# Optimization experiments

Measured on AMD Instinct MI355X. Metric: run time of the kernel, lower is better.

The kernel has to match this reference:

```python
import jax, jax.numpy as jnp
import numpy as np

NQ, NS, QN, SN = 10000, 500, 4, 10   # num_question, num_skill, q/s neighbor sizes
B, S, D = 32, 200, 128               # batch, seq_len, emb_dim
HOPS = 3


def setup_inputs() -> dict:
    key = jax.random.key(0)
    ks = iter(jax.random.split(key, 40))

    def nrm(shape, scale=0.05):
        return jax.random.normal(next(ks), shape, dtype=jnp.float32) * scale

    return {
        "question": jax.random.randint(next(ks), (B, S), 0, NQ),
        "response": jax.random.randint(next(ks), (B, S), 0, 2),
        "mask": jnp.ones((B, S), dtype=jnp.int32),
        "q_neighbors": jax.random.randint(next(ks), (NQ, QN), 0, NS),  # question -> skill ids
        "s_neighbors": jax.random.randint(next(ks), (NS, SN), 0, NQ),  # skill -> question ids
        "qs_skills": jax.random.randint(next(ks), (NQ, 4), 0, NS),     # related skills per question
        "emb_q": nrm((NQ, D), 1.0),
        "emb_s": nrm((NS, D), 1.0),
        "emb_r": nrm((2, D), 1.0),
        "W_ih": nrm((2 * D, 4 * D)), "b_ih": nrm((4 * D,)), "b_hh": nrm((4 * D,)),
        "ft_W": nrm((D, D)), "ft_b": nrm((D,)),
        "agg_W": nrm((HOPS, D, D)), "agg_b": nrm((HOPS, D)),
        "last_W": nrm((D, D)), "last_b": nrm((D,)),
        "q_W": nrm((D, D)), "q_b": nrm((D,)),
        "k_W": nrm((D, D)), "k_b": nrm((D,)),
        "w_W": nrm((2 * D,)), "w_b": nrm(()),
    }


def reference(question, response, mask, q_neighbors, s_neighbors, qs_skills,
              emb_q, emb_s, emb_r, W_ih, b_ih, b_hh, ft_W, ft_b,
              agg_W, agg_b, last_W, last_b, q_W, q_b, k_W, k_b, w_W, w_b):
    # ---- multi-hop GNN aggregation for every (b, t) question (mask == 1 everywhere) ----
    q_flat = question.reshape(-1)              # [B*S]
    lvl1 = q_neighbors[q_flat]                 # [N, QN]            skill ids
    lvl2 = s_neighbors[lvl1]                   # [N, QN, SN]        question ids
    lvl3 = q_neighbors[lvl2]                   # [N, QN, SN, QN]    skill ids
    embs = [emb_q[q_flat], emb_s[lvl1], emb_q[lvl2], emb_s[lvl3]]
    for i in range(HOPS):
        embs = [jnp.tanh((embs[j] + embs[j + 1].mean(axis=-2)) @ agg_W[j] + agg_b[j])
                for j in range(HOPS - i)]
    agg_emb = jnp.tanh(embs[0] @ last_W + last_b).reshape(B, S, D)

    # ---- per-step input + zero-state LSTMCell (source calls lstm_cell without hx) ----
    q_trans = jax.nn.relu(agg_emb @ ft_W + ft_b)
    x = jnp.concatenate([q_trans, emb_r[response]], axis=-1)   # [B, S, 2D]
    gates = x @ W_ih + b_ih + b_hh                             # h_prev = 0, c_prev = 0
    i_g, f_g, g_g, o_g = jnp.split(gates, 4, axis=-1)
    c = jax.nn.sigmoid(i_g) * jnp.tanh(g_g)
    h = jax.nn.sigmoid(o_g) * jnp.tanh(c)                      # [B, S, D]
    states = h[:, :S - 1]                                      # state written at step t

    # ---- soft-recap attention prediction for q_next = question[:, t+1] ----
    q_next = question[:, 1:]                                   # [B, T], T = S-1
    qs = jnp.concatenate([emb_q[q_next][:, :, None, :], emb_s[qs_skills[q_next]]], axis=2)  # [B,T,5,D]

    inner = jnp.einsum('bnd,btmd->btnm', states, qs)           # state/qs inner products
    a_state = (states @ q_W + q_b) @ w_W[:D]                   # [B, N]  MLP_query on states
    a_qs = (qs @ k_W + k_b) @ w_W[D:]                          # [B, T, 5] MLP_key on qs
    logits = a_state[:, None, :, None] + a_qs[:, :, None, :] + w_b  # [B, T, N, 5]

    t_idx = jnp.arange(S - 1)
    valid = t_idx[None, :] <= t_idx[:, None]                   # [T, N]: states 0..t visible at t
    logits = jnp.where(valid[None, :, :, None], logits, -jnp.inf)
    alpha = jax.nn.softmax(logits.reshape(B, S - 1, -1), axis=-1).reshape(logits.shape)
    pred = jnp.sum(alpha * jax.nn.sigmoid(inner), axis=(2, 3))  # [B, T]

    return jnp.zeros((B, S), jnp.float32).at[:, 1:].set(pred)
```

## Files before the change

kernel.cpp:

```cpp
#include <hip/hip_runtime.h>

typedef unsigned short u16;
typedef unsigned int   u32;

#define NQd 10000
#define NSd 500
#define Bd  32
#define Sd  200
#define Td  199
#define Dd  128
#define NR  6368
#define PB  208

typedef __attribute__((ext_vector_type(8))) short bf16x8;
typedef __attribute__((ext_vector_type(4))) float f32x4;

__device__ __forceinline__ float sigf(float x) {
  return __builtin_amdgcn_rcpf(1.f + __expf(-x));
}
__device__ __forceinline__ float tanh_f(float x) {
  float ax = fminf(fabsf(x), 15.f);
  float e = __expf(2.f * ax);
  float r = 1.f - 2.f * __builtin_amdgcn_rcpf(e + 1.f);
  return copysignf(r, x);
}
__device__ __forceinline__ float bf2f(u16 u) { return __uint_as_float(((u32)u) << 16); }
__device__ __forceinline__ u16 f2bf(float f) {
  u32 b = __float_as_uint(f);
  b += 0x7FFFu + ((b >> 16) & 1u);
  return (u16)(b >> 16);
}
__device__ __forceinline__ float rnd(float x) { return bf2f(f2bf(x)); }
__device__ __forceinline__ void unp2(u32 u, float &a, float &b) {
  a = __uint_as_float(u << 16);
  b = __uint_as_float(u & 0xffff0000u);
}
__device__ __forceinline__ void unpack16(uint4 a0, uint4 a1, float* f) {
  unp2(a0.x, f[0], f[1]);  unp2(a0.y, f[2], f[3]);
  unp2(a0.z, f[4], f[5]);  unp2(a0.w, f[6], f[7]);
  unp2(a1.x, f[8], f[9]);  unp2(a1.y, f[10], f[11]);
  unp2(a1.z, f[12], f[13]); unp2(a1.w, f[14], f[15]);
}

struct Args {
  const int *question, *response, *q_nb, *s_nb, *qs_sk;
  const float *emb_q, *emb_s, *emb_r;
  const float *W_ih, *b_ih, *b_hh, *ft_W, *ft_b, *agg_W, *agg_b, *last_W, *last_b;
  const float *q_W, *q_b, *k_W, *k_b, *w_W;
  u16 *tabA, *tabB, *tabs1, *tabs2, *states, *embq_bf, *embs_bf, *wts, *wiht;
  float *a_state, *qw, *kw, *scal, *er_part, *pm;
  int *qid_map, *resp_map, *flag, *cnt, *gflag, *list, *newidx;
};

struct WF { bf16x8 v[2][4]; };

__device__ __forceinline__ void load_WF(const u16* Wt, int l15, int quad, int cw, WF& w)
{
#pragma unroll
  for (int nt = 0; nt < 2; ++nt)
#pragma unroll
    for (int kc = 0; kc < 4; ++kc)
      w.v[nt][kc] = *(const bf16x8*)&Wt[(long)(cw + nt * 16 + l15) * 128 + kc * 32 + quad * 8];
}

__device__ __forceinline__ void load_WF_f32(const float* W, int l15, int quad, int cw, WF& w)
{
#pragma unroll
  for (int nt = 0; nt < 2; ++nt) {
    int col = cw + nt * 16 + l15;
#pragma unroll
    for (int kc = 0; kc < 4; ++kc) {
      int kb = kc * 32 + quad * 8;
      bf16x8 t;
#pragma unroll
      for (int j = 0; j < 8; ++j) t[j] = (short)f2bf(W[(long)(kb + j) * 128 + col]);
      w.v[nt][kc] = t;
    }
  }
}

__device__ __forceinline__ void zero_acc(f32x4 acc[2][2]) {
#pragma unroll
  for (int x = 0; x < 2; ++x)
#pragma unroll
    for (int y = 0; y < 2; ++y) acc[x][y] = (f32x4){0.f, 0.f, 0.f, 0.f};
}

__device__ __forceinline__ void mfma_WF(const u16* Al, const WF& w,
                                        int l15, int quad, f32x4 acc[2][2])
{
#pragma unroll
  for (int kc = 0; kc < 4; ++kc) {
    const int ko = kc * 32 + quad * 8;
    bf16x8 a0 = *(const bf16x8*)&Al[l15 * 136 + ko];
    bf16x8 a1 = *(const bf16x8*)&Al[(16 + l15) * 136 + ko];
    acc[0][0] = __builtin_amdgcn_mfma_f32_16x16x32_bf16(a0, w.v[0][kc], acc[0][0], 0, 0, 0);
    acc[0][1] = __builtin_amdgcn_mfma_f32_16x16x32_bf16(a0, w.v[1][kc], acc[0][1], 0, 0, 0);
    acc[1][0] = __builtin_amdgcn_mfma_f32_16x16x32_bf16(a1, w.v[0][kc], acc[1][0], 0, 0, 0);
    acc[1][1] = __builtin_amdgcn_mfma_f32_16x16x32_bf16(a1, w.v[1][kc], acc[1][1], 0, 0, 0);
  }
}

__device__ __forceinline__ void stage_A(const u16* Atab, const u16* Btab,
                                        const int* nbr, int K, const int* rowmap,
                                        int tile0, int rows, int tid, u16* Al)
{
  int r = tid & 31, k0 = (tid >> 5) * 16;
  int row = tile0 + r; if (row >= rows) row = rows - 1;
  int arow = rowmap ? rowmap[row] : row;
  const u16* ap = Atab + (long)arow * 128 + k0;
  if (K == 0) {
    *(uint4*)&Al[r * 136 + k0]     = *(const uint4*)ap;
    *(uint4*)&Al[r * 136 + k0 + 8] = *(const uint4*)(ap + 8);
  } else {
    float f[16];
    unpack16(*(const uint4*)ap, *(const uint4*)(ap + 8), f);
    float s[16];
#pragma unroll
    for (int q = 0; q < 16; ++q) s[q] = 0.f;
    for (int l = 0; l < K; ++l) {
      int id = nbr[(long)arow * K + l];
      const u16* np = Btab + (long)id * 128 + k0;
      float g[16];
      unpack16(*(const uint4*)np, *(const uint4*)(np + 8), g);
#pragma unroll
      for (int q = 0; q < 16; ++q) s[q] += g[q];
    }
    float inv = 1.f / (float)K;
#pragma unroll
    for (int q = 0; q < 16; ++q) f[q] += s[q] * inv;
    u32 p[8];
#pragma unroll
    for (int q = 0; q < 8; ++q)
      p[q] = (u32)f2bf(f[2 * q]) | ((u32)f2bf(f[2 * q + 1]) << 16);
    *(uint4*)&Al[r * 136 + k0]     = make_uint4(p[0], p[1], p[2], p[3]);
    *(uint4*)&Al[r * 136 + k0 + 8] = make_uint4(p[4], p[5], p[6], p[7]);
  }
}

__device__ __forceinline__ void ld16_rnd(const float* p, float* f)
{
#pragma unroll
  for (int q4 = 0; q4 < 4; ++q4) {
    float4 v = *(const float4*)(p + q4 * 4);
    f[q4 * 4 + 0] = rnd(v.x); f[q4 * 4 + 1] = rnd(v.y);
    f[q4 * 4 + 2] = rnd(v.z); f[q4 * 4 + 3] = rnd(v.w);
  }
}

__device__ __forceinline__ void stage_A_f32(const float* Atab, const float* Btab,
                                            const int* nbr, int K,
                                            int tile0, int rows, int tid, u16* Al)
{
  int r = tid & 31, k0 = (tid >> 5) * 16;
  int row = tile0 + r; if (row >= rows) row = rows - 1;
  float f[16];
  ld16_rnd(Atab + (long)row * 128 + k0, f);
  float s[16];
#pragma unroll
  for (int q = 0; q < 16; ++q) s[q] = 0.f;
  for (int l = 0; l < K; ++l) {
    int id = nbr[(long)row * K + l];
    float g[16];
    ld16_rnd(Btab + (long)id * 128 + k0, g);
#pragma unroll
    for (int q = 0; q < 16; ++q) s[q] += g[q];
  }
  float inv = 1.f / (float)K;
#pragma unroll
  for (int q = 0; q < 16; ++q) f[q] += s[q] * inv;
  u32 p[8];
#pragma unroll
  for (int q = 0; q < 8; ++q)
    p[q] = (u32)f2bf(f[2 * q]) | ((u32)f2bf(f[2 * q + 1]) << 16);
  *(uint4*)&Al[r * 136 + k0]     = make_uint4(p[0], p[1], p[2], p[3]);
  *(uint4*)&Al[r * 136 + k0 + 8] = make_uint4(p[4], p[5], p[6], p[7]);
}

__device__ __forceinline__ void update_A(const u16* Btab, const int* nbr,
                                         const int* rowmap, int tile0, int rows,
                                         int tid, u16* Al)
{
  int r = tid & 31, k0 = (tid >> 5) * 16;
  int row = tile0 + r; if (row >= rows) row = rows - 1;
  int arow = rowmap ? rowmap[row] : row;
  float f[16];
  unpack16(*(const uint4*)&Al[r * 136 + k0], *(const uint4*)&Al[r * 136 + k0 + 8], f);
  float s[16];
#pragma unroll
  for (int q = 0; q < 16; ++q) s[q] = 0.f;
#pragma unroll
  for (int l = 0; l < 4; ++l) {
    int id = nbr[(long)arow * 4 + l];
    const u16* np = Btab + (long)id * 128 + k0;
    float g[16];
    unpack16(*(const uint4*)np, *(const uint4*)(np + 8), g);
#pragma unroll
    for (int q = 0; q < 16; ++q) s[q] += g[q];
  }
#pragma unroll
  for (int q = 0; q < 16; ++q) f[q] += s[q] * 0.25f;
  u32 p[8];
#pragma unroll
  for (int q = 0; q < 8; ++q)
    p[q] = (u32)f2bf(f[2 * q]) | ((u32)f2bf(f[2 * q + 1]) << 16);
  *(uint4*)&Al[r * 136 + k0]     = make_uint4(p[0], p[1], p[2], p[3]);
  *(uint4*)&Al[r * 136 + k0 + 8] = make_uint4(p[4], p[5], p[6], p[7]);
}

__device__ __forceinline__ void epi_tanh_global(const f32x4 acc[2][2], const float* cbias,
                                                u16* out, int rows, int tile0,
                                                int l15, int quad, int cw)
{
#pragma unroll
  for (int nt = 0; nt < 2; ++nt) {
    int col = cw + nt * 16 + l15;
    float cb = cbias[col];
#pragma unroll
    for (int mt = 0; mt < 2; ++mt) {
      int rbase = tile0 + mt * 16 + quad * 4;
#pragma unroll
      for (int i = 0; i < 4; ++i) {
        int row = rbase + i;
        if (row >= rows) continue;
        out[(long)row * 128 + col] = f2bf(tanh_f(acc[mt][nt][i] + cb));
      }
    }
  }
}

__device__ __forceinline__ void epi_tanh_lds(const f32x4 acc[2][2], const float* cbias,
                                             u16* Al, int l15, int quad, int cw)
{
#pragma unroll
  for (int nt = 0; nt < 2; ++nt) {
    int col = cw + nt * 16 + l15;
    float cb = cbias[col];
#pragma unroll
    for (int mt = 0; mt < 2; ++mt)
#pragma unroll
      for (int i = 0; i < 4; ++i) {
        int rL = mt * 16 + quad * 4 + i;
        Al[rL * 136 + col] = f2bf(tanh_f(acc[mt][nt][i] + cb));
      }
  }
}

__global__ __launch_bounds__(256) void prep2(Args a, float* __restrict__ out)
{
  __shared__ __align__(16) u16 Al[32 * 136];
  const int i = blockIdx.x, tid = threadIdx.x;
  const int lane = tid & 63, wv = tid >> 6;
  const int l15 = lane & 15, quad = lane >> 4, cw = wv * 32;

  if (i < 313) {
    const int tile0 = i * 32;
    WF w2, w0;
    load_WF_f32(a.agg_W + 2 * 16384, l15, quad, cw, w2);
    load_WF_f32(a.agg_W, l15, quad, cw, w0);
    stage_A_f32(a.emb_q, a.emb_s, a.q_nb, 4, tile0, NQd, tid, Al);
    __syncthreads();
    f32x4 acc[2][2];
    zero_acc(acc);
    mfma_WF(Al, w2, l15, quad, acc);
    epi_tanh_global(acc, a.agg_b + 256, a.tabA, NQd, tile0, l15, quad, cw);
    zero_acc(acc);
    mfma_WF(Al, w0, l15, quad, acc);
    epi_tanh_global(acc, a.agg_b, a.tabB, NQd, tile0, l15, quad, cw);
    return;
  }
  if (i < 329) {
    const int tile0 = (i - 313) * 32;
    WF w1;
    load_WF_f32(a.agg_W + 16384, l15, quad, cw, w1);
    stage_A_f32(a.emb_s, a.emb_q, a.s_nb, 10, tile0, NSd, tid, Al);
    __syncthreads();
    f32x4 acc[2][2];
    zero_acc(acc);
    mfma_WF(Al, w1, l15, quad, acc);
    epi_tanh_global(acc, a.agg_b + 128, a.tabs1, NSd, tile0, l15, quad, cw);
    return;
  }

  const int T = 640 * 256;
  for (int j = (i - 329) * 256 + tid; j < 497506; j += T) {
    if (j < 320000) {
      float4 v = *(const float4*)&a.emb_q[(long)j * 4];
      ((uint2*)a.embq_bf)[j] = make_uint2(
          (u32)f2bf(v.x) | ((u32)f2bf(v.y) << 16),
          (u32)f2bf(v.z) | ((u32)f2bf(v.w) << 16));
    } else if (j < 336000) {
      int c = j - 320000;
      float4 v = *(const float4*)&a.emb_s[(long)c * 4];
      ((uint2*)a.embs_bf)[c] = make_uint2(
          (u32)f2bf(v.x) | ((u32)f2bf(v.y) << 16),
          (u32)f2bf(v.z) | ((u32)f2bf(v.w) << 16));
    } else if (j < 417920) {
      int e = j - 336000;
      int seg = e >> 14, r = e & 16383;
      int col = r >> 7, k = r & 127;
      const float* src = (seg < 3) ? (a.agg_W + seg * 16384)
                                   : (seg == 3 ? a.last_W : a.ft_W);
      a.wts[e] = f2bf(src[k * 128 + col]);
    } else if (j < 483456) {
      int e = j - 417920;
      int col = e >> 7, k = e & 127;
      a.wiht[e] = f2bf(a.W_ih[k * 512 + col]);
    } else if (j < 489824) {
      int jj = j - 483456;
      int b = jj / Td, s = jj - b * Td;
      int qid = a.question[b * Sd + s];
      a.qid_map[jj]  = qid;
      a.resp_map[jj] = a.response[b * Sd + s];
      if (atomicExch(&a.flag[qid], 1) == 0) {
        int idx = atomicAdd(a.cnt, 1);
        a.list[idx] = qid;
        a.newidx[qid] = idx;
      }
    } else if (j < 491106) {
      int s = j - 489824;
      if (s < 128) {
        float acc = 0;
        for (int e = 0; e < 128; ++e) acc += a.q_W[s * 128 + e] * a.w_W[e];
        a.qw[s] = acc;
      } else if (s < 256) {
        int d = s - 128; float acc = 0;
        for (int e = 0; e < 128; ++e) acc += a.k_W[d * 128 + e] * a.w_W[128 + e];
        a.kw[d] = acc;
      } else if (s == 256) {
        float acc = 0;
        for (int e = 0; e < 128; ++e) acc += a.q_b[e] * a.w_W[e];
        a.scal[0] = acc;
      } else if (s == 257) {
        float acc = 0;
        for (int e = 0; e < 128; ++e) acc += a.k_b[e] * a.w_W[128 + e];
        a.scal[1] = acc;
      } else {
        int e2 = s - 258, rr = e2 >> 9, col = e2 & 511;
        float acc = a.b_ih[col] + a.b_hh[col];
        for (int d = 0; d < 128; ++d) acc += a.emb_r[rr * Dd + d] * a.W_ih[(128 + d) * 512 + col];
        a.er_part[rr * 512 + col] = acc;
      }
    } else {
      out[j - 491106] = 0.f;
    }
  }
}

__global__ __launch_bounds__(256) void chain4m(Args a)
{
  __shared__ __align__(16) u16 Al[32 * 136];
  const int i = blockIdx.x, tid = threadIdx.x;
  const int lane = tid & 63, wv = tid >> 6;
  const int l15 = lane & 15, quad = lane >> 4, cw = wv * 32;

  if (i < 16) {
    const int tile0 = i * 32;
    WF w1; load_WF(a.wts + 16384, l15, quad, cw, w1);
    stage_A(a.tabs1, a.tabA, a.s_nb, 10, nullptr, tile0, NSd, tid, Al);
    __syncthreads();
    f32x4 acc[2][2];
    zero_acc(acc);
    mfma_WF(Al, w1, l15, quad, acc);
    epi_tanh_global(acc, a.agg_b + 128, a.tabs2, NSd, tile0, l15, quad, cw);
    __syncthreads();
    if (tid == 0)
      __hip_atomic_fetch_add(a.gflag, 1, __ATOMIC_RELEASE, __HIP_MEMORY_SCOPE_AGENT);
    return;
  }

  if (i < 41) {
    int item = (i - 16) * 256 + tid;
    if (item >= NR) return;
    int b = item / Td, t = item - b * Td;
    int qn = a.question[b * Sd + t + 1];
    float am[5];
#pragma unroll
    for (int m = 0; m < 5; ++m) {
      const u16* src = (m == 0) ? a.embq_bf + (long)qn * 128
                                : a.embs_bf + (long)a.qs_sk[qn * 4 + (m - 1)] * 128;
      float s = 0.f;
      for (int k = 0; k < 128; k += 8) {
        uint4 u = *(const uint4*)&src[k];
        float f[8];
        unp2(u.x, f[0], f[1]); unp2(u.y, f[2], f[3]);
        unp2(u.z, f[4], f[5]); unp2(u.w, f[6], f[7]);
#pragma unroll
        for (int q = 0; q < 8; ++q) s = fmaf(f[q], a.kw[k + q], s);
      }
      am[m] = s + a.scal[1];
    }
    float mx = am[0];
#pragma unroll
    for (int m = 1; m < 5; ++m) mx = fmaxf(mx, am[m]);
    float ex[5], z = 0.f;
#pragma unroll
    for (int m = 0; m < 5; ++m) { ex[m] = __expf(am[m] - mx); z += ex[m]; }
    float iz = __builtin_amdgcn_rcpf(z);
#pragma unroll
    for (int m = 0; m < 5; ++m) a.pm[((long)b * PB + t) * 5 + m] = ex[m] * iz;
    return;
  }

  const int cnt = *a.cnt;
  const int tile0 = (i - 41) * 32;
  if (tile0 >= cnt) return;
  WF w0, w3, w4;
  load_WF(a.wts, l15, quad, cw, w0);
  load_WF(a.wts + 3 * 16384, l15, quad, cw, w3);
  load_WF(a.wts + 4 * 16384, l15, quad, cw, w4);
  f32x4 acc[2][2];

  stage_A(a.tabB, a.tabs1, a.q_nb, 4, a.list, tile0, cnt, tid, Al);
  __syncthreads();
  zero_acc(acc);
  mfma_WF(Al, w0, l15, quad, acc);
  __syncthreads();
  epi_tanh_lds(acc, a.agg_b, Al, l15, quad, cw);
  __syncthreads();
  if (tid == 0) {
    while (__hip_atomic_load(a.gflag, __ATOMIC_ACQUIRE, __HIP_MEMORY_SCOPE_AGENT) < 16) {}
  }
  __syncthreads();
  update_A(a.tabs2, a.q_nb, a.list, tile0, cnt, tid, Al);
  __syncthreads();
  zero_acc(acc);
  mfma_WF(Al, w0, l15, quad, acc);
  __syncthreads();
  epi_tanh_lds(acc, a.agg_b, Al, l15, quad, cw);
  __syncthreads();
  zero_acc(acc);
  mfma_WF(Al, w3, l15, quad, acc);
  __syncthreads();
  epi_tanh_lds(acc, a.last_b, Al, l15, quad, cw);
  __syncthreads();
  zero_acc(acc);
  mfma_WF(Al, w4, l15, quad, acc);
#pragma unroll
  for (int nt = 0; nt < 2; ++nt) {
    int col = cw + nt * 16 + l15;
    float cb = a.ft_b[col];
#pragma unroll
    for (int mt = 0; mt < 2; ++mt) {
      int rbase = tile0 + mt * 16 + quad * 4;
#pragma unroll
      for (int i2 = 0; i2 < 4; ++i2) {
        int row = rbase + i2;
        if (row >= cnt) continue;
        a.tabA[(long)row * 128 + col] = f2bf(fmaxf(acc[mt][nt][i2] + cb, 0.f));
      }
    }
  }
}

__global__ __launch_bounds__(256) void gates_k(Args a)
{
  __shared__ __align__(16) u16 Al[32 * 136];
  __shared__ float hb[32 * 132];
  const int tid = threadIdx.x;
  const int lane = tid & 63, wv = tid >> 6;
  const int l15 = lane & 15, quad = lane >> 4, cw = wv * 32;

  const int tile0 = blockIdx.x * 32;
  WF wg0, wg1, wg2;
  load_WF(a.wiht, l15, quad, cw, wg0);
  load_WF(a.wiht + (long)256 * 128, l15, quad, cw, wg1);
  load_WF(a.wiht + (long)384 * 128, l15, quad, cw, wg2);
  {
    int r = tid & 31, k0 = (tid >> 5) * 16;
    int row = tile0 + r;
    int arow = a.newidx[a.qid_map[row]];
    const u16* ap = a.tabA + (long)arow * 128 + k0;
    *(uint4*)&Al[r * 136 + k0]     = *(const uint4*)ap;
    *(uint4*)&Al[r * 136 + k0 + 8] = *(const uint4*)(ap + 8);
  }
  __syncthreads();
  f32x4 acc[3][2][2];
  zero_acc(acc[0]); mfma_WF(Al, wg0, l15, quad, acc[0]);
  zero_acc(acc[1]); mfma_WF(Al, wg1, l15, quad, acc[1]);
  zero_acc(acc[2]); mfma_WF(Al, wg2, l15, quad, acc[2]);
#pragma unroll
  for (int nt = 0; nt < 2; ++nt) {
    int colL = cw + nt * 16 + l15;
#pragma unroll
    for (int mt = 0; mt < 2; ++mt) {
#pragma unroll
      for (int i = 0; i < 4; ++i) {
        int rL = mt * 16 + quad * 4 + i;
        int row = tile0 + rL;
        const float* rb = a.er_part + (long)a.resp_map[row] * 512;
        float iv = acc[0][mt][nt][i] + rb[colL];
        float gv = acc[1][mt][nt][i] + rb[256 + colL];
        float ov = acc[2][mt][nt][i] + rb[384 + colL];
        float c = sigf(iv) * tanh_f(gv);
        float h = sigf(ov) * tanh_f(c);
        a.states[(long)row * 128 + colL] = f2bf(h);
        hb[rL * 132 + colL] = h;
      }
    }
  }
  __syncthreads();
#pragma unroll
  for (int rr = 0; rr < 8; ++rr) {
    int rL = wv * 8 + rr;
    float p = hb[rL * 132 + lane] * a.qw[lane] + hb[rL * 132 + 64 + lane] * a.qw[64 + lane];
#pragma unroll
    for (int off = 32; off > 0; off >>= 1) p += __shfl_xor(p, off);
    if (lane == 0) a.a_state[tile0 + rL] = p + a.scal[0];
  }
}

__global__ __launch_bounds__(256) void gk_pred(Args a, float* __restrict__ out)
{
  static const int cys[14]   = {0,1,2,3,3,4,4,5,5,6,6,7,7,7};
  static const int nx0s[14]  = {0,0,0,0,3,0,3,0,3,0,3,0,3,6};
  static const int ncnts[14] = {1,2,3,3,1,3,1,3,2,3,3,3,3,1};
  const int chunk = blockIdx.x, b = blockIdx.y;
  const int cy = cys[chunk], nx0 = nx0s[chunk], ncnt = ncnts[chunk];
  const int c0 = cy * 128;
  int c_hi = c0 + 127; if (c_hi > 994) c_hi = 994;
  const int tmax = c_hi / 5, tmin = c0 / 5;

  __shared__ __align__(16) u16 smem[21760];
  __shared__ float predl[32];
  __shared__ float evl[256];
  __shared__ float scl[256];
  u16* Ql = smem;
  u16* Sl = smem + 17408;
  const int tid = threadIdx.x;

  float v = (tid < Td) ? a.a_state[b * Td + tid] : -1e30f;
  scl[tid] = v; __syncthreads();
  for (int s = 128; s > 0; s >>= 1) { if (tid < s) scl[tid] = fmaxf(scl[tid], scl[tid + s]); __syncthreads(); }
  float gmax = scl[0]; __syncthreads();
  float e = (tid < Td) ? __expf(v - gmax) : 0.f;
  evl[tid] = e;
  scl[tid] = e;
  if (tid < 32) predl[tid] = 0.f;
  __syncthreads();
  for (int off = 1; off < 256; off <<= 1) {
    float add = (tid >= off) ? scl[tid - off] : 0.f;
    __syncthreads();
    scl[tid] += add;
    __syncthreads();
  }

  {
    int j = tid >> 1, k0 = (tid & 1) * 64;
    int col = c0 + j;
    uint4* dst = (uint4*)&Ql[j * 136 + k0];
    if (col < 995) {
      int t = col / 5, m = col - t * 5;
      int qn = a.question[b * Sd + t + 1];
      const u16* src = (m == 0) ? a.embq_bf + (long)qn * 128
                                : a.embs_bf + (long)a.qs_sk[qn * 4 + (m - 1)] * 128;
      src += k0;
#pragma unroll
      for (int q = 0; q < 8; ++q) dst[q] = ((const uint4*)src)[q];
    } else {
      uint4 z = make_uint4(0, 0, 0, 0);
#pragma unroll
      for (int q = 0; q < 8; ++q) dst[q] = z;
    }
  }

  const int lane = tid & 63, wv = tid >> 6;
  const int l15 = lane & 15, quad = lane >> 4, cw = wv * 32;

  for (int xi = 0; xi < ncnt; ++xi) {
    const int n0 = (nx0 + xi) * 32;
    __syncthreads();
    {
      int r = tid & 31, k0 = (tid >> 5) * 16;
      int n = n0 + r; if (n > 198) n = 198;
      const u16* sp = a.states + ((long)b * Td + n) * 128 + k0;
      *(uint4*)&Sl[r * 136 + k0]     = *(const uint4*)sp;
      *(uint4*)&Sl[r * 136 + k0 + 8] = *(const uint4*)(sp + 8);
    }
    __syncthreads();
    f32x4 acc[2][2];
    zero_acc(acc);
#pragma unroll
    for (int kc = 0; kc < 4; ++kc) {
      const int ko = kc * 32 + quad * 8;
      bf16x8 af[2], bfv[2];
      af[0]  = *(const bf16x8*)&Sl[l15 * 136 + ko];
      af[1]  = *(const bf16x8*)&Sl[(16 + l15) * 136 + ko];
      bfv[0] = *(const bf16x8*)&Ql[(cw + l15) * 136 + ko];
      bfv[1] = *(const bf16x8*)&Ql[(cw + 16 + l15) * 136 + ko];
#pragma unroll
      for (int mt = 0; mt < 2; ++mt)
#pragma unroll
        for (int nt = 0; nt < 2; ++nt)
          acc[mt][nt] = __builtin_amdgcn_mfma_f32_16x16x32_bf16(af[mt], bfv[nt], acc[mt][nt], 0, 0, 0);
    }

#pragma unroll
    for (int nt = 0; nt < 2; ++nt) {
      int col = c0 + cw + nt * 16 + l15;
      if (col >= 995) continue;
      int t = col / 5, m = col - t * 5;
      float pmv = a.pm[((long)b * PB + t) * 5 + m];
      float part = 0.f;
#pragma unroll
      for (int mt = 0; mt < 2; ++mt) {
        int nb = n0 + mt * 16 + quad * 4;
        if (nb > t) continue;
#pragma unroll
        for (int i = 0; i < 4; ++i) {
          int n = nb + i;
          if (n > t || n > 198) continue;
          part += evl[n] * sigf(acc[mt][nt][i]);
        }
      }
      part *= pmv;
      if (part != 0.f) atomicAdd(&predl[t - tmin], part);
    }
  }
  __syncthreads();
  const int tcnt = tmax - tmin + 1;
  if (tid < tcnt) {
    int t = tmin + tid;
    float pv = predl[tid];
    if (pv != 0.f)
      atomicAdd(&out[b * Sd + t + 1], pv * (1.f / scl[t]));
  }
}

extern "C" void kernel_launch(void* const* d_in, const int* in_sizes, int n_in,
                              void* d_out, int out_size, void* d_ws, size_t ws_size,
                              hipStream_t stream)
{
  Args a;
  a.question = (const int*)d_in[0];
  a.response = (const int*)d_in[1];
  a.q_nb     = (const int*)d_in[3];
  a.s_nb     = (const int*)d_in[4];
  a.qs_sk    = (const int*)d_in[5];
  a.emb_q    = (const float*)d_in[6];
  a.emb_s    = (const float*)d_in[7];
  a.emb_r    = (const float*)d_in[8];
  a.W_ih     = (const float*)d_in[9];
  a.b_ih     = (const float*)d_in[10];
  a.b_hh     = (const float*)d_in[11];
  a.ft_W     = (const float*)d_in[12];
  a.ft_b     = (const float*)d_in[13];
  a.agg_W    = (const float*)d_in[14];
  a.agg_b    = (const float*)d_in[15];
  a.last_W   = (const float*)d_in[16];
  a.last_b   = (const float*)d_in[17];
  a.q_W      = (const float*)d_in[18];
  a.q_b      = (const float*)d_in[19];
  a.k_W      = (const float*)d_in[20];
  a.k_b      = (const float*)d_in[21];
  a.w_W      = (const float*)d_in[22];

  u16* wsu = (u16*)d_ws;
  const long NT = 1280000, ST = 64000, RT = (long)NR * Dd;
  a.tabA  = wsu;
  a.tabB  = a.tabA + NT;
  a.tabs1 = a.tabB + NT;
  a.tabs2 = a.tabs1 + ST;
  a.states  = a.tabs2 + ST;
  a.embq_bf = a.states + RT;
  a.embs_bf = a.embq_bf + NT;
  a.wts     = a.embs_bf + ST;
  a.wiht    = a.wts + 5 * 16384;
  float* fp = (float*)(a.wiht + 65536);
  a.a_state = fp;
  a.qw      = fp + 6368;
  a.kw      = fp + 6496;
  a.scal    = fp + 6624;
  a.er_part = fp + 6640;
  a.pm      = fp + 7664;
  a.qid_map  = (int*)(a.pm + 32 * PB * 5);
  a.resp_map = a.qid_map + NR;
  a.flag     = a.resp_map + NR;
  a.cnt      = a.flag + NQd;
  a.gflag    = a.cnt + 1;
  a.list     = a.cnt + 4;
  a.newidx   = a.list + NQd;

  float* out = (float*)d_out;

  hipMemsetAsync(a.flag, 0, (NQd + 4) * sizeof(int), stream);
  prep2<<<969, 256, 0, stream>>>(a, out);
  chain4m<<<240, 256, 0, stream>>>(a);
  gates_k<<<199, 256, 0, stream>>>(a);
  gk_pred<<<dim3(14, Bd), 256, 0, stream>>>(a, out);
}
```

Baseline: 168.5 us.

## Merge GNN chain and LSTM gate kernels into one flag-synchronised kernel

Combines the GNN chain kernel and the LSTM gates kernel into one 471-block launch. Blocks hand off work through global atomic counters: gates blocks spin until all 199 chain blocks finish, and 32 new blocks wait on the gates counter. Those 32 blocks compute the per-batch softmax max, exponentials and prefix-sum normalisers once and store them in a workspace, so the 14 prediction blocks per batch stop recomputing them. The aim is to remove a kernel launch boundary and redundant reductions. It relies on producer blocks being scheduled before spinning consumers, which risks deadlock or idle spinning if occupancy is insufficient.

```diff
diff --git a/kernel.cpp b/kernel.cpp
--- a/kernel.cpp
+++ b/kernel.cpp
@@ -48,8 +48,8 @@
   const float *W_ih, *b_ih, *b_hh, *ft_W, *ft_b, *agg_W, *agg_b, *last_W, *last_b;
   const float *q_W, *q_b, *k_W, *k_b, *w_W;
   u16 *tabA, *tabB, *tabs1, *tabs2, *states, *embq_bf, *embs_bf, *wts, *wiht;
-  float *a_state, *qw, *kw, *scal, *er_part, *pm;
-  int *qid_map, *resp_map, *flag, *cnt, *gflag, *list, *newidx;
+  float *a_state, *qw, *kw, *scal, *er_part, *ev, *invZ, *pm;
+  int *qid_map, *resp_map, *flag, *cnt, *gflag, *cflag, *sflag, *list, *newidx;
 };
 
 struct WF { bf16x8 v[2][4]; };
@@ -347,9 +347,10 @@
   }
 }
 
-__global__ __launch_bounds__(256) void chain4m(Args a)
+__global__ __launch_bounds__(256, 2) void mega2(Args a)
 {
   __shared__ __align__(16) u16 Al[32 * 136];
+  __shared__ float hb[32 * 132];
   const int i = blockIdx.x, tid = threadIdx.x;
   const int lane = tid & 63, wv = tid >> 6;
   const int l15 = lane & 15, quad = lane >> 4, cw = wv * 32;
@@ -402,111 +403,144 @@
     return;
   }
 
-  const int cnt = *a.cnt;
-  const int tile0 = (i - 41) * 32;
-  if (tile0 >= cnt) return;
-  WF w0, w3, w4;
-  load_WF(a.wts, l15, quad, cw, w0);
-  load_WF(a.wts + 3 * 16384, l15, quad, cw, w3);
-  load_WF(a.wts + 4 * 16384, l15, quad, cw, w4);
-  f32x4 acc[2][2];
-
-  stage_A(a.tabB, a.tabs1, a.q_nb, 4, a.list, tile0, cnt, tid, Al);
-  __syncthreads();
-  zero_acc(acc);
-  mfma_WF(Al, w0, l15, quad, acc);
-  __syncthreads();
-  epi_tanh_lds(acc, a.agg_b, Al, l15, quad, cw);
-  __syncthreads();
-  if (tid == 0) {
-    while (__hip_atomic_load(a.gflag, __ATOMIC_ACQUIRE, __HIP_MEMORY_SCOPE_AGENT) < 16) {}
-  }
-  __syncthreads();
-  update_A(a.tabs2, a.q_nb, a.list, tile0, cnt, tid, Al);
-  __syncthreads();
-  zero_acc(acc);
-  mfma_WF(Al, w0, l15, quad, acc);
-  __syncthreads();
-  epi_tanh_lds(acc, a.agg_b, Al, l15, quad, cw);
-  __syncthreads();
-  zero_acc(acc);
-  mfma_WF(Al, w3, l15, quad, acc);
-  __syncthreads();
-  epi_tanh_lds(acc, a.last_b, Al, l15, quad, cw);
-  __syncthreads();
-  zero_acc(acc);
-  mfma_WF(Al, w4, l15, quad, acc);
-#pragma unroll
-  for (int nt = 0; nt < 2; ++nt) {
-    int col = cw + nt * 16 + l15;
-    float cb = a.ft_b[col];
-#pragma unroll
-    for (int mt = 0; mt < 2; ++mt) {
-      int rbase = tile0 + mt * 16 + quad * 4;
-#pragma unroll
-      for (int i2 = 0; i2 < 4; ++i2) {
-        int row = rbase + i2;
-        if (row >= cnt) continue;
-        a.tabA[(long)row * 128 + col] = f2bf(fmaxf(acc[mt][nt][i2] + cb, 0.f));
-      }
-    }
-  }
-}
-
-__global__ __launch_bounds__(256) void gates_k(Args a)
-{
-  __shared__ __align__(16) u16 Al[32 * 136];
-  __shared__ float hb[32 * 132];
-  const int tid = threadIdx.x;
-  const int lane = tid & 63, wv = tid >> 6;
-  const int l15 = lane & 15, quad = lane >> 4, cw = wv * 32;
-
-  const int tile0 = blockIdx.x * 32;
-  WF wg0, wg1, wg2;
-  load_WF(a.wiht, l15, quad, cw, wg0);
-  load_WF(a.wiht + (long)256 * 128, l15, quad, cw, wg1);
-  load_WF(a.wiht + (long)384 * 128, l15, quad, cw, wg2);
+  if (i < 240) {
+    const int cnt = *a.cnt;
+    const int tile0 = (i - 41) * 32;
+    if (tile0 < cnt) {
+      WF w0, w3, w4;
+      load_WF(a.wts, l15, quad, cw, w0);
+      load_WF(a.wts + 3 * 16384, l15, quad, cw, w3);
+      load_WF(a.wts + 4 * 16384, l15, quad, cw, w4);
+      f32x4 acc[2][2];
+
+      stage_A(a.tabB, a.tabs1, a.q_nb, 4, a.list, tile0, cnt, tid, Al);
+      __syncthreads();
+      zero_acc(acc);
+      mfma_WF(Al, w0, l15, quad, acc);
+      __syncthreads();
+      epi_tanh_lds(acc, a.agg_b, Al, l15, quad, cw);
+      __syncthreads();
+      if (tid == 0) {
+        while (__hip_atomic_load(a.gflag, __ATOMIC_ACQUIRE, __HIP_MEMORY_SCOPE_AGENT) < 16) {}
+      }
+      __syncthreads();
+      update_A(a.tabs2, a.q_nb, a.list, tile0, cnt, tid, Al);
+      __syncthreads();
+      zero_acc(acc);
+      mfma_WF(Al, w0, l15, quad, acc);
+      __syncthreads();
+      epi_tanh_lds(acc, a.agg_b, Al, l15, quad, cw);
+      __syncthreads();
+      zero_acc(acc);
+      mfma_WF(Al, w3, l15, quad, acc);
+      __syncthreads();
+      epi_tanh_lds(acc, a.last_b, Al, l15, quad, cw);
+      __syncthreads();
+      zero_acc(acc);
+      mfma_WF(Al, w4, l15, quad, acc);
+#pragma unroll
+      for (int nt = 0; nt < 2; ++nt) {
+        int col = cw + nt * 16 + l15;
+        float cb = a.ft_b[col];
+#pragma unroll
+        for (int mt = 0; mt < 2; ++mt) {
+          int rbase = tile0 + mt * 16 + quad * 4;
+#pragma unroll
+          for (int i2 = 0; i2 < 4; ++i2) {
+            int row = rbase + i2;
+            if (row >= cnt) continue;
+            a.tabA[(long)row * 128 + col] = f2bf(fmaxf(acc[mt][nt][i2] + cb, 0.f));
+          }
+        }
+      }
+      __syncthreads();
+    }
+    if (tid == 0)
+      __hip_atomic_fetch_add(a.cflag, 1, __ATOMIC_RELEASE, __HIP_MEMORY_SCOPE_AGENT);
+    return;
+  }
+
+  if (i < 439) {
+    const int tile0 = (i - 240) * 32;
+    WF wg0, wg1, wg2;
+    load_WF(a.wiht, l15, quad, cw, wg0);
+    load_WF(a.wiht + (long)256 * 128, l15, quad, cw, wg1);
+    load_WF(a.wiht + (long)384 * 128, l15, quad, cw, wg2);
+    if (tid == 0) {
+      while (__hip_atomic_load(a.cflag, __ATOMIC_ACQUIRE, __HIP_MEMORY_SCOPE_AGENT) < 199) {}
+    }
+    __syncthreads();
+    {
+      int r = tid & 31, k0 = (tid >> 5) * 16;
+      int row = tile0 + r;
+      int arow = a.newidx[a.qid_map[row]];
+      const u16* ap = a.tabA + (long)arow * 128 + k0;
+      *(uint4*)&Al[r * 136 + k0]     = *(const uint4*)ap;
+      *(uint4*)&Al[r * 136 + k0 + 8] = *(const uint4*)(ap + 8);
+    }
+    __syncthreads();
+    f32x4 acc[3][2][2];
+    zero_acc(acc[0]); mfma_WF(Al, wg0, l15, quad, acc[0]);
+    zero_acc(acc[1]); mfma_WF(Al, wg1, l15, quad, acc[1]);
+    zero_acc(acc[2]); mfma_WF(Al, wg2, l15, quad, acc[2]);
+#pragma unroll
+    for (int nt = 0; nt < 2; ++nt) {
+      int colL = cw + nt * 16 + l15;
+#pragma unroll
+      for (int mt = 0; mt < 2; ++mt) {
+#pragma unroll
+        for (int i2 = 0; i2 < 4; ++i2) {
+          int rL = mt * 16 + quad * 4 + i2;
+          int row = tile0 + rL;
+          const float* rb = a.er_part + (long)a.resp_map[row] * 512;
+          float iv = acc[0][mt][nt][i2] + rb[colL];
+          float gv = acc[1][mt][nt][i2] + rb[256 + colL];
+          float ov = acc[2][mt][nt][i2] + rb[384 + colL];
+          float c = sigf(iv) * tanh_f(gv);
+          float h = sigf(ov) * tanh_f(c);
+          a.states[(long)row * 128 + colL] = f2bf(h);
+          hb[rL * 132 + colL] = h;
+        }
+      }
+    }
+    __syncthreads();
+#pragma unroll
+    for (int rr = 0; rr < 8; ++rr) {
+      int rL = wv * 8 + rr;
+      float p = hb[rL * 132 + lane] * a.qw[lane] + hb[rL * 132 + 64 + lane] * a.qw[64 + lane];
+#pragma unroll
+      for (int off = 32; off > 0; off >>= 1) p += __shfl_xor(p, off);
+      if (lane == 0) a.a_state[tile0 + rL] = p + a.scal[0];
+    }
+    __syncthreads();
+    if (tid == 0)
+      __hip_atomic_fetch_add(a.sflag, 1, __ATOMIC_RELEASE, __HIP_MEMORY_SCOPE_AGENT);
+    return;
+  }
+
   {
-    int r = tid & 31, k0 = (tid >> 5) * 16;
-    int row = tile0 + r;
-    int arow = a.newidx[a.qid_map[row]];
-    const u16* ap = a.tabA + (long)arow * 128 + k0;
-    *(uint4*)&Al[r * 136 + k0]     = *(const uint4*)ap;
-    *(uint4*)&Al[r * 136 + k0 + 8] = *(const uint4*)(ap + 8);
-  }
-  __syncthreads();
-  f32x4 acc[3][2][2];
-  zero_acc(acc[0]); mfma_WF(Al, wg0, l15, quad, acc[0]);
-  zero_acc(acc[1]); mfma_WF(Al, wg1, l15, quad, acc[1]);
-  zero_acc(acc[2]); mfma_WF(Al, wg2, l15, quad, acc[2]);
-#pragma unroll
-  for (int nt = 0; nt < 2; ++nt) {
-    int colL = cw + nt * 16 + l15;
-#pragma unroll
-    for (int mt = 0; mt < 2; ++mt) {
-#pragma unroll
-      for (int i = 0; i < 4; ++i) {
-        int rL = mt * 16 + quad * 4 + i;
-        int row = tile0 + rL;
-        const float* rb = a.er_part + (long)a.resp_map[row] * 512;
-        float iv = acc[0][mt][nt][i] + rb[colL];
-        float gv = acc[1][mt][nt][i] + rb[256 + colL];
-        float ov = acc[2][mt][nt][i] + rb[384 + colL];
-        float c = sigf(iv) * tanh_f(gv);
-        float h = sigf(ov) * tanh_f(c);
-        a.states[(long)row * 128 + colL] = f2bf(h);
-        hb[rL * 132 + colL] = h;
-      }
-    }
-  }
-  __syncthreads();
-#pragma unroll
-  for (int rr = 0; rr < 8; ++rr) {
-    int rL = wv * 8 + rr;
-    float p = hb[rL * 132 + lane] * a.qw[lane] + hb[rL * 132 + 64 + lane] * a.qw[64 + lane];
-#pragma unroll
-    for (int off = 32; off > 0; off >>= 1) p += __shfl_xor(p, off);
-    if (lane == 0) a.a_state[tile0 + rL] = p + a.scal[0];
+    const int b = i - 439;
+    float* red = hb;
+    float* evl = hb + 256;
+    if (tid == 0) {
+      while (__hip_atomic_load(a.sflag, __ATOMIC_ACQUIRE, __HIP_MEMORY_SCOPE_AGENT) < 199) {}
+    }
+    __syncthreads();
+    float v = (tid < Td) ? a.a_state[b * Td + tid] : -1e30f;
+    red[tid] = v; __syncthreads();
+    for (int s = 128; s > 0; s >>= 1) { if (tid < s) red[tid] = fmaxf(red[tid], red[tid + s]); __syncthreads(); }
+    float gmax = red[0]; __syncthreads();
+    float e = (tid < Td) ? __expf(v - gmax) : 0.f;
+    evl[tid] = e;
+    if (tid < Td) a.ev[b * PB + tid] = e;
+    __syncthreads();
+    for (int off = 1; off < 256; off <<= 1) {
+      float add = (tid >= off) ? evl[tid - off] : 0.f;
+      __syncthreads();
+      evl[tid] += add;
+      __syncthreads();
+    }
+    if (tid < Td) a.invZ[b * PB + tid] = 1.f / evl[tid];
   }
 }
 
@@ -524,26 +558,12 @@
   __shared__ __align__(16) u16 smem[21760];
   __shared__ float predl[32];
   __shared__ float evl[256];
-  __shared__ float scl[256];
   u16* Ql = smem;
   u16* Sl = smem + 17408;
   const int tid = threadIdx.x;
 
-  float v = (tid < Td) ? a.a_state[b * Td + tid] : -1e30f;
-  scl[tid] = v; __syncthreads();
-  for (int s = 128; s > 0; s >>= 1) { if (tid < s) scl[tid] = fmaxf(scl[tid], scl[tid + s]); __syncthreads(); }
-  float gmax = scl[0]; __syncthreads();
-  float e = (tid < Td) ? __expf(v - gmax) : 0.f;
-  evl[tid] = e;
-  scl[tid] = e;
+  evl[tid] = (tid < Td) ? a.ev[b * PB + tid] : 0.f;
   if (tid < 32) predl[tid] = 0.f;
-  __syncthreads();
-  for (int off = 1; off < 256; off <<= 1) {
-    float add = (tid >= off) ? scl[tid - off] : 0.f;
-    __syncthreads();
-    scl[tid] += add;
-    __syncthreads();
-  }
 
   {
     int j = tid >> 1, k0 = (tid & 1) * 64;
@@ -623,7 +643,7 @@
     int t = tmin + tid;
     float pv = predl[tid];
     if (pv != 0.f)
-      atomicAdd(&out[b * Sd + t + 1], pv * (1.f / scl[t]));
+      atomicAdd(&out[b * Sd + t + 1], pv * a.invZ[b * PB + t]);
   }
 }
 
@@ -672,12 +692,16 @@
   a.kw      = fp + 6496;
   a.scal    = fp + 6624;
   a.er_part = fp + 6640;
-  a.pm      = fp + 7664;
+  a.ev      = fp + 7664;
+  a.invZ    = a.ev + 32 * PB;
+  a.pm      = a.invZ + 32 * PB;
   a.qid_map  = (int*)(a.pm + 32 * PB * 5);
   a.resp_map = a.qid_map + NR;
   a.flag     = a.resp_map + NR;
   a.cnt      = a.flag + NQd;
   a.gflag    = a.cnt + 1;
+  a.cflag    = a.cnt + 2;
+  a.sflag    = a.cnt + 3;
   a.list     = a.cnt + 4;
   a.newidx   = a.list + NQd;
 
@@ -685,7 +709,6 @@
 
   hipMemsetAsync(a.flag, 0, (NQd + 4) * sizeof(int), stream);
   prep2<<<969, 256, 0, stream>>>(a, out);
-  chain4m<<<240, 256, 0, stream>>>(a);
-  gates_k<<<199, 256, 0, stream>>>(a);
+  mega2<<<471, 256, 0, stream>>>(a);
   gk_pred<<<dim3(14, Bd), 256, 0, stream>>>(a, out);
 }
```

After: 261.8 us. 55.4% more time.
